# Kernel tuning notes

Hardware: AMD Instinct MI355X
Metric: run time of the kernel (lower is better)

Reference implementation:

```python
import jax, jax.numpy as jnp
import numpy as np

ED = 1024
NH = 16
HD = ED // NH


def setup_inputs() -> dict:
    key = jax.random.key(0)
    ks = jax.random.split(key, 9)
    s = 1.0 / np.sqrt(ED)
    return {
        "x": jax.random.normal(ks[0], (2, 2048, ED), dtype=jnp.float32),
        "wq": jax.random.uniform(ks[1], (ED, ED), jnp.float32, -s, s),
        "bq": jax.random.uniform(ks[2], (ED,), jnp.float32, -s, s),
        "wk": jax.random.uniform(ks[3], (ED, ED), jnp.float32, -s, s),
        "bk": jax.random.uniform(ks[4], (ED,), jnp.float32, -s, s),
        "wv": jax.random.uniform(ks[5], (ED, ED), jnp.float32, -s, s),
        "bv": jax.random.uniform(ks[6], (ED,), jnp.float32, -s, s),
        "wo": jax.random.uniform(ks[7], (ED, ED), jnp.float32, -s, s),
        "bo": jax.random.uniform(ks[8], (ED,), jnp.float32, -s, s),
    }


def reference(x, wq, bq, wk, bk, wv, bv, wo, bo):
    B, N, _ = x.shape
    # projections; weights stored as [out, in] like nn.Linear -> x @ W.T + b
    def proj(w, b):
        y = jnp.einsum('bnd,ed->bne', x, w) + b
        return y.reshape(B, N, NH, HD).transpose(0, 2, 1, 3)  # [B, H, N, hd]
    Q, K, V = proj(wq, bq), proj(wk, bk), proj(wv, bv)
    scores = jnp.einsum('bhnd,bhmd->bhnm', Q, K) / jnp.sqrt(jnp.float32(HD))
    attn = jax.nn.softmax(scores, axis=-1)
    ctx = jnp.einsum('bhnm,bhmd->bhnd', attn, V)
    ctx = ctx.transpose(0, 2, 1, 3).reshape(B, N, ED)
    return jnp.einsum('bne,de->bnd', ctx, wo) + bo
```

## Files before the change

### kernel.cpp

```cpp
#include <hip/hip_runtime.h>
#include <hip/hip_bf16.h>

#define ED 1024
#define NH 16
#define HD 64
#define SEQ 2048

typedef float f32x4 __attribute__((ext_vector_type(4)));
typedef short s16x8 __attribute__((ext_vector_type(8)));
typedef short s16x4 __attribute__((ext_vector_type(4)));
typedef __attribute__((address_space(1))) const unsigned int GBuf;
typedef __attribute__((address_space(3))) unsigned int LBuf;

#define QSC 0.18033688011112042f

union BF8 { s16x8 v; __hip_bfloat16 h[8]; };

__device__ inline void cvt_one(const float* __restrict__ s, __hip_bfloat16* __restrict__ d,
                               int n, int t, int stride) {
  const int n8 = n >> 3;
  for (int i = t; i < n8; i += stride) {
    const float4 u = ((const float4*)s)[2 * i];
    const float4 v = ((const float4*)s)[2 * i + 1];
    BF8 o;
    o.h[0] = __float2bfloat16(u.x); o.h[1] = __float2bfloat16(u.y);
    o.h[2] = __float2bfloat16(u.z); o.h[3] = __float2bfloat16(u.w);
    o.h[4] = __float2bfloat16(v.x); o.h[5] = __float2bfloat16(v.y);
    o.h[6] = __float2bfloat16(v.z); o.h[7] = __float2bfloat16(v.w);
    ((s16x8*)d)[i] = o.v;
  }
}

__global__ __launch_bounds__(256) void cvt5(const float* s0, const float* s1, const float* s2,
                                            const float* s3, const float* s4,
                                            __hip_bfloat16* d0, __hip_bfloat16* d1,
                                            __hip_bfloat16* d2, __hip_bfloat16* d3,
                                            __hip_bfloat16* d4,
                                            int n0, int n1, int n2, int n3, int n4) {
  const int stride = gridDim.x * blockDim.x;
  const int t = blockIdx.x * blockDim.x + threadIdx.x;
  cvt_one(s0, d0, n0, t, stride);
  cvt_one(s1, d1, n1, t, stride);
  cvt_one(s2, d2, n2, t, stride);
  cvt_one(s3, d3, n3, t, stride);
  cvt_one(s4, d4, n4, t, stride);
}

__global__ __launch_bounds__(256) void gemm_qkv(const __hip_bfloat16* __restrict__ A,
                                                const __hip_bfloat16* __restrict__ wq,
                                                const float* __restrict__ bq,
                                                const __hip_bfloat16* __restrict__ wk,
                                                const float* __restrict__ bk,
                                                const __hip_bfloat16* __restrict__ wv,
                                                const float* __restrict__ bv,
                                                __hip_bfloat16* __restrict__ Qo,
                                                __hip_bfloat16* __restrict__ Ko,
                                                __hip_bfloat16* __restrict__ Vo) {
  __shared__ __hip_bfloat16 As[128 * 64];
  __shared__ __hip_bfloat16 Bs[128 * 64];

  const int z = blockIdx.z;
  const __hip_bfloat16* W = (z == 0) ? wq : (z == 1) ? wk : wv;
  const float* bias = (z == 0) ? bq : (z == 1) ? bk : bv;

  const int tid = threadIdx.x;
  const int wave = tid >> 6, lane = tid & 63;
  const int ln15 = lane & 15, lg = lane >> 4;
  const int m0 = blockIdx.y * 128, n0 = blockIdx.x * 128;
  const int wr = (wave >> 1) * 64, wc = (wave & 1) * 64;

  f32x4 acc[4][4];
#pragma unroll
  for (int i = 0; i < 4; i++)
#pragma unroll
    for (int j = 0; j < 4; j++) acc[i][j] = (f32x4){0.f, 0.f, 0.f, 0.f};

  const int srow = tid >> 3;
  const int sk = (tid & 7) * 8;

  for (int k0 = 0; k0 < ED; k0 += 64) {
    __syncthreads();
#pragma unroll
    for (int c = 0; c < 4; c++) {
      const int r = c * 32 + srow;
      __builtin_amdgcn_global_load_lds((GBuf*)(A + (size_t)(m0 + r) * ED + k0 + sk),
                                       (LBuf*)((char*)As + c * 4096 + tid * 16), 16, 0, 0);
    }
#pragma unroll
    for (int c = 0; c < 4; c++) {
      const int r = c * 32 + srow;
      __builtin_amdgcn_global_load_lds((GBuf*)(W + (size_t)(n0 + r) * ED + k0 + sk),
                                       (LBuf*)((char*)Bs + c * 4096 + tid * 16), 16, 0, 0);
    }
    __syncthreads();
#pragma unroll
    for (int kb = 0; kb < 2; kb++) {
      const int kof = kb * 32 + lg * 8;
      s16x8 a[4], b[4];
#pragma unroll
      for (int i = 0; i < 4; i++)
        a[i] = *(const s16x8*)&As[(wr + i * 16 + ln15) * 64 + kof];
#pragma unroll
      for (int j = 0; j < 4; j++)
        b[j] = *(const s16x8*)&Bs[(wc + j * 16 + ln15) * 64 + kof];
#pragma unroll
      for (int i = 0; i < 4; i++)
#pragma unroll
        for (int j = 0; j < 4; j++)
          acc[i][j] = __builtin_amdgcn_mfma_f32_16x16x32_bf16(a[i], b[j], acc[i][j], 0, 0, 0);
    }
  }

  const float scale = (z == 0) ? QSC : 1.0f;
  if (z < 2) {
    __hip_bfloat16* out = (z == 0) ? Qo : Ko;
#pragma unroll
    for (int j = 0; j < 4; j++) {
      const int e = n0 + wc + j * 16 + ln15;
      const float bvv = bias[e];
      const int h = e >> 6, hd = e & 63;
#pragma unroll
      for (int i = 0; i < 4; i++) {
#pragma unroll
        for (int r = 0; r < 4; r++) {
          const int m = m0 + wr + i * 16 + lg * 4 + r;
          const int b = m >> 11, n = m & 2047;
          out[(((size_t)(b * NH + h)) * SEQ + n) * HD + hd] =
              __float2bfloat16((acc[i][j][r] + bvv) * scale);
        }
      }
    }
  } else {
#pragma unroll
    for (int j = 0; j < 4; j++) {
      const int e = n0 + wc + j * 16 + ln15;
      const float bvv = bias[e];
      const int h = e >> 6, hd = e & 63;
#pragma unroll
      for (int i = 0; i < 4; i++) {
        const int m = m0 + wr + i * 16 + lg * 4;
        const int b = m >> 11, n = m & 2047;
        union { s16x4 v; __hip_bfloat16 hh[4]; } pk;
#pragma unroll
        for (int r = 0; r < 4; r++) pk.hh[r] = __float2bfloat16(acc[i][j][r] + bvv);
        *(s16x4*)&Vo[(((size_t)(b * NH + h)) * HD + hd) * SEQ + n] = pk.v;
      }
    }
  }
}

__global__ __launch_bounds__(256) void gemm_out(const __hip_bfloat16* __restrict__ A,
                                                const __hip_bfloat16* __restrict__ W,
                                                const float* __restrict__ bias,
                                                float* __restrict__ out) {
  __shared__ __hip_bfloat16 As[128 * 64];
  __shared__ __hip_bfloat16 Bs[128 * 64];

  const int tid = threadIdx.x;
  const int wave = tid >> 6, lane = tid & 63;
  const int ln15 = lane & 15, lg = lane >> 4;
  const int m0 = blockIdx.y * 128, n0 = blockIdx.x * 128;
  const int wr = (wave >> 1) * 64, wc = (wave & 1) * 64;

  f32x4 acc[4][4];
#pragma unroll
  for (int i = 0; i < 4; i++)
#pragma unroll
    for (int j = 0; j < 4; j++) acc[i][j] = (f32x4){0.f, 0.f, 0.f, 0.f};

  const int srow = tid >> 3;
  const int sk = (tid & 7) * 8;

  for (int k0 = 0; k0 < ED; k0 += 64) {
    __syncthreads();
#pragma unroll
    for (int c = 0; c < 4; c++) {
      const int r = c * 32 + srow;
      __builtin_amdgcn_global_load_lds((GBuf*)(A + (size_t)(m0 + r) * ED + k0 + sk),
                                       (LBuf*)((char*)As + c * 4096 + tid * 16), 16, 0, 0);
    }
#pragma unroll
    for (int c = 0; c < 4; c++) {
      const int r = c * 32 + srow;
      __builtin_amdgcn_global_load_lds((GBuf*)(W + (size_t)(n0 + r) * ED + k0 + sk),
                                       (LBuf*)((char*)Bs + c * 4096 + tid * 16), 16, 0, 0);
    }
    __syncthreads();
#pragma unroll
    for (int kb = 0; kb < 2; kb++) {
      const int kof = kb * 32 + lg * 8;
      s16x8 a[4], b[4];
#pragma unroll
      for (int i = 0; i < 4; i++)
        a[i] = *(const s16x8*)&As[(wr + i * 16 + ln15) * 64 + kof];
#pragma unroll
      for (int j = 0; j < 4; j++)
        b[j] = *(const s16x8*)&Bs[(wc + j * 16 + ln15) * 64 + kof];
#pragma unroll
      for (int i = 0; i < 4; i++)
#pragma unroll
        for (int j = 0; j < 4; j++)
          acc[i][j] = __builtin_amdgcn_mfma_f32_16x16x32_bf16(a[i], b[j], acc[i][j], 0, 0, 0);
    }
  }

#pragma unroll
  for (int j = 0; j < 4; j++) {
    const int e = n0 + wc + j * 16 + ln15;
    const float bvv = bias[e];
#pragma unroll
    for (int i = 0; i < 4; i++)
#pragma unroll
      for (int r = 0; r < 4; r++) {
        const int m = m0 + wr + i * 16 + lg * 4 + r;
        out[(size_t)m * ED + e] = acc[i][j][r] + bvv;
      }
  }
}

__global__ __launch_bounds__(256) void attn_bf16(const __hip_bfloat16* __restrict__ Q,
                                                 const __hip_bfloat16* __restrict__ K,
                                                 const __hip_bfloat16* __restrict__ VT,
                                                 __hip_bfloat16* __restrict__ CTX) {
  __shared__ __hip_bfloat16 Ks[64 * 64];
  __shared__ __hip_bfloat16 Vt[64 * 64];
  __shared__ __hip_bfloat16 Ps[4 * 32 * 64];

  const int tid = threadIdx.x;
  const int wave = tid >> 6, lane = tid & 63;
  const int ln15 = lane & 15, lg = lane >> 4;
  const unsigned swz = (unsigned)((ln15 & 7) << 4);

  const int bid = blockIdx.x;
  const int work = (bid & 7) * 64 + (bid >> 3);
  const int qb = work & 15;
  const int bh = work >> 4;

  const __hip_bfloat16* Qh = Q + (size_t)bh * SEQ * HD;
  const __hip_bfloat16* Kh = K + (size_t)bh * SEQ * HD;
  const __hip_bfloat16* Vh = VT + (size_t)bh * HD * SEQ;
  __hip_bfloat16* Pw = Ps + wave * 32 * 64;

  s16x8 aq[2][2];
#pragma unroll
  for (int qs = 0; qs < 2; qs++) {
    const int qrow = qb * 128 + wave * 32 + qs * 16 + ln15;
#pragma unroll
    for (int kb = 0; kb < 2; kb++)
      aq[qs][kb] = *(const s16x8*)&Qh[(size_t)qrow * HD + kb * 32 + lg * 8];
  }

  f32x4 acc_o[2][4];
#pragma unroll
  for (int qs = 0; qs < 2; qs++)
#pragma unroll
    for (int db = 0; db < 4; db++) acc_o[qs][db] = (f32x4){0.f, 0.f, 0.f, 0.f};
  float m_[2] = {-1e30f, -1e30f};
  float l_[2] = {0.f, 0.f};

  for (int kt = 0; kt < SEQ / 64; kt++) {
    __syncthreads();
#pragma unroll
    for (int c = 0; c < 2; c++) {
      const int row = c * 32 + (tid >> 3);
      const int colb = ((tid & 7) * 16) ^ ((row & 7) << 4);
      __builtin_amdgcn_global_load_lds(
          (GBuf*)((const char*)Kh + ((size_t)(kt * 64 + row) * HD) * 2 + colb),
          (LBuf*)((char*)Ks + c * 4096 + tid * 16), 16, 0, 0);
      __builtin_amdgcn_global_load_lds(
          (GBuf*)((const char*)Vh + ((size_t)row * SEQ + kt * 64) * 2 + colb),
          (LBuf*)((char*)Vt + c * 4096 + tid * 16), 16, 0, 0);
    }
    __syncthreads();

    f32x4 s[2][4];
#pragma unroll
    for (int qs = 0; qs < 2; qs++)
#pragma unroll
      for (int cb = 0; cb < 4; cb++) s[qs][cb] = (f32x4){0.f, 0.f, 0.f, 0.f};
#pragma unroll
    for (int cb = 0; cb < 4; cb++) {
      const int krow = cb * 16 + ln15;
#pragma unroll
      for (int kb = 0; kb < 2; kb++) {
        const s16x8 ak =
            *(const s16x8*)((const char*)Ks + krow * 128 + ((kb * 64 + lg * 16) ^ swz));
#pragma unroll
        for (int qs = 0; qs < 2; qs++)
          s[qs][cb] = __builtin_amdgcn_mfma_f32_16x16x32_bf16(ak, aq[qs][kb], s[qs][cb], 0, 0, 0);
      }
    }

#pragma unroll
    for (int qs = 0; qs < 2; qs++) {
      float tm = -1e30f;
#pragma unroll
      for (int cb = 0; cb < 4; cb++)
        tm = fmaxf(tm, fmaxf(fmaxf(s[qs][cb][0], s[qs][cb][1]),
                             fmaxf(s[qs][cb][2], s[qs][cb][3])));
      tm = fmaxf(tm, __shfl_xor(tm, 16));
      tm = fmaxf(tm, __shfl_xor(tm, 32));
      const float mnew = fmaxf(m_[qs], tm);
      const float fs = exp2f(m_[qs] - mnew);
      m_[qs] = mnew;
      float sum = 0.f;
#pragma unroll
      for (int cb = 0; cb < 4; cb++)
#pragma unroll
        for (int r = 0; r < 4; r++) {
          const float p = exp2f(s[qs][cb][r] - mnew);
          s[qs][cb][r] = p;
          sum += p;
        }
      sum += __shfl_xor(sum, 16);
      sum += __shfl_xor(sum, 32);
      l_[qs] = l_[qs] * fs + sum;
#pragma unroll
      for (int db = 0; db < 4; db++)
#pragma unroll
        for (int r = 0; r < 4; r++) acc_o[qs][db][r] *= fs;
      const int prow = qs * 16 + ln15;
#pragma unroll
      for (int cb = 0; cb < 4; cb++)
#pragma unroll
        for (int r = 0; r < 4; r++) {
          const int kv2 = (cb * 16 + lg * 4 + r) * 2;
          *(__hip_bfloat16*)((char*)Pw + prow * 128 + (kv2 ^ swz)) =
              __float2bfloat16(s[qs][cb][r]);
        }
    }

#pragma unroll
    for (int kb = 0; kb < 2; kb++) {
      s16x8 bp[2];
#pragma unroll
      for (int qs = 0; qs < 2; qs++) {
        const int prow = qs * 16 + ln15;
        bp[qs] = *(const s16x8*)((const char*)Pw + prow * 128 + ((kb * 64 + lg * 16) ^ swz));
      }
#pragma unroll
      for (int db = 0; db < 4; db++) {
        const int vrow = db * 16 + ln15;
        const s16x8 av =
            *(const s16x8*)((const char*)Vt + vrow * 128 + ((kb * 64 + lg * 16) ^ swz));
#pragma unroll
        for (int qs = 0; qs < 2; qs++)
          acc_o[qs][db] = __builtin_amdgcn_mfma_f32_16x16x32_bf16(av, bp[qs], acc_o[qs][db], 0, 0, 0);
      }
    }
  }

  const int b = bh / NH, h = bh % NH;
#pragma unroll
  for (int qs = 0; qs < 2; qs++) {
    const float inv = 1.0f / l_[qs];
    const int n = qb * 128 + wave * 32 + qs * 16 + ln15;
    __hip_bfloat16* dst = &CTX[((size_t)(b * SEQ + n)) * ED + h * HD + lg * 4];
#pragma unroll
    for (int db = 0; db < 4; db++) {
      union { s16x4 v; __hip_bfloat16 hh[4]; } pk;
#pragma unroll
      for (int r = 0; r < 4; r++) pk.hh[r] = __float2bfloat16(acc_o[qs][db][r] * inv);
      *(s16x4*)&dst[db * 16] = pk.v;
    }
  }
}

extern "C" void kernel_launch(void* const* d_in, const int* in_sizes, int n_in,
                              void* d_out, int out_size, void* d_ws, size_t ws_size,
                              hipStream_t stream) {
  const float* x = (const float*)d_in[0];
  const float* wq = (const float*)d_in[1];
  const float* bq = (const float*)d_in[2];
  const float* wk = (const float*)d_in[3];
  const float* bk = (const float*)d_in[4];
  const float* wv = (const float*)d_in[5];
  const float* bv = (const float*)d_in[6];
  const float* wo = (const float*)d_in[7];
  const float* bo = (const float*)d_in[8];
  float* out = (float*)d_out;

  const int BN = in_sizes[0] / ED;

  char* w = (char*)d_ws;
  __hip_bfloat16* xbf = (__hip_bfloat16*)(w);
  __hip_bfloat16* wqb = (__hip_bfloat16*)(w + (8 << 20));
  __hip_bfloat16* wkb = (__hip_bfloat16*)(w + (10 << 20));
  __hip_bfloat16* wvb = (__hip_bfloat16*)(w + (12 << 20));
  __hip_bfloat16* wob = (__hip_bfloat16*)(w + (14 << 20));
  __hip_bfloat16* Qb = (__hip_bfloat16*)(w + (16 << 20));
  __hip_bfloat16* Kb = (__hip_bfloat16*)(w + (24 << 20));
  __hip_bfloat16* VTb = (__hip_bfloat16*)(w + (32 << 20));
  __hip_bfloat16* CTXb = (__hip_bfloat16*)(w + (40 << 20));

  cvt5<<<1024, 256, 0, stream>>>(x, wq, wk, wv, wo, xbf, wqb, wkb, wvb, wob,
                                 BN * ED, ED * ED, ED * ED, ED * ED, ED * ED);

  const dim3 blk(256);
  gemm_qkv<<<dim3(ED / 128, BN / 128, 3), blk, 0, stream>>>(
      xbf, wqb, bq, wkb, bk, wvb, bv, Qb, Kb, VTb);

  attn_bf16<<<dim3(512), blk, 0, stream>>>(Qb, Kb, VTb, CTXb);

  gemm_out<<<dim3(ED / 128, BN / 128), blk, 0, stream>>>(CTXb, wob, bo, out);
}
```

Measured before the change: 263.6 us.

## Rewrite attention inner loop with 32x32 MFMA, register P, double-buffered K/V

The attention kernel switches from 16x16x32 to 32x32x16 bf16 MFMA tiles. The softmax probabilities are packed into B-fragments in registers with v_cvt_pk_bf16 and v_permlane32_swap instead of a round trip through LDS. K/V tiles are now double-buffered so the next tile's global-to-LDS load overlaps compute, which removes one barrier per iteration. Rescaling of the running max is skipped unless the max grows by more than 8 (a lazy rescale), which trades a little numerical headroom for fewer multiplies on the accumulators.

```diff
diff --git a/kernel.cpp b/kernel.cpp
--- a/kernel.cpp
+++ b/kernel.cpp
@@ -7,6 +7,7 @@
 #define SEQ 2048
 
 typedef float f32x4 __attribute__((ext_vector_type(4)));
+typedef float f32x16 __attribute__((ext_vector_type(16)));
 typedef short s16x8 __attribute__((ext_vector_type(8)));
 typedef short s16x4 __attribute__((ext_vector_type(4)));
 typedef __attribute__((address_space(1))) const unsigned int GBuf;
@@ -15,6 +16,23 @@
 #define QSC 0.18033688011112042f
 
 union BF8 { s16x8 v; __hip_bfloat16 h[8]; };
+
+__device__ __forceinline__ unsigned cvt_pk_bf16(float lo, float hi) {
+  unsigned r;
+  asm("v_cvt_pk_bf16_f32 %0, %1, %2" : "=v"(r) : "v"(lo), "v"(hi));
+  return r;
+}
+
+__device__ __forceinline__ s16x8 pack_pfrag(float p0, float p1, float p2, float p3,
+                                            float p4, float p5, float p6, float p7) {
+  unsigned w0 = cvt_pk_bf16(p0, p1), w1 = cvt_pk_bf16(p2, p3);
+  unsigned w2 = cvt_pk_bf16(p4, p5), w3 = cvt_pk_bf16(p6, p7);
+  asm("v_permlane32_swap_b32 %0, %1" : "+v"(w0), "+v"(w2));
+  asm("v_permlane32_swap_b32 %0, %1" : "+v"(w1), "+v"(w3));
+  union { unsigned u[4]; s16x8 v; } r;
+  r.u[0] = w0; r.u[1] = w1; r.u[2] = w2; r.u[3] = w3;
+  return r.v;
+}
 
 __device__ inline void cvt_one(const float* __restrict__ s, __hip_bfloat16* __restrict__ d,
                                int n, int t, int stride) {
@@ -222,14 +240,13 @@
                                                  const __hip_bfloat16* __restrict__ K,
                                                  const __hip_bfloat16* __restrict__ VT,
                                                  __hip_bfloat16* __restrict__ CTX) {
-  __shared__ __hip_bfloat16 Ks[64 * 64];
-  __shared__ __hip_bfloat16 Vt[64 * 64];
-  __shared__ __hip_bfloat16 Ps[4 * 32 * 64];
+  __shared__ __hip_bfloat16 KsS[2][64 * 64];
+  __shared__ __hip_bfloat16 VtS[2][64 * 64];
 
   const int tid = threadIdx.x;
   const int wave = tid >> 6, lane = tid & 63;
-  const int ln15 = lane & 15, lg = lane >> 4;
-  const unsigned swz = (unsigned)((ln15 & 7) << 4);
+  const int l31 = lane & 31, hi = lane >> 5;
+  const int rswz = l31 & 7;
 
   const int bid = blockIdx.x;
   const int work = (bid & 7) * 64 + (bid >> 3);
@@ -239,130 +256,108 @@
   const __hip_bfloat16* Qh = Q + (size_t)bh * SEQ * HD;
   const __hip_bfloat16* Kh = K + (size_t)bh * SEQ * HD;
   const __hip_bfloat16* Vh = VT + (size_t)bh * HD * SEQ;
-  __hip_bfloat16* Pw = Ps + wave * 32 * 64;
-
-  s16x8 aq[2][2];
-#pragma unroll
-  for (int qs = 0; qs < 2; qs++) {
-    const int qrow = qb * 128 + wave * 32 + qs * 16 + ln15;
-#pragma unroll
-    for (int kb = 0; kb < 2; kb++)
-      aq[qs][kb] = *(const s16x8*)&Qh[(size_t)qrow * HD + kb * 32 + lg * 8];
-  }
-
-  f32x4 acc_o[2][4];
-#pragma unroll
-  for (int qs = 0; qs < 2; qs++)
-#pragma unroll
-    for (int db = 0; db < 4; db++) acc_o[qs][db] = (f32x4){0.f, 0.f, 0.f, 0.f};
-  float m_[2] = {-1e30f, -1e30f};
-  float l_[2] = {0.f, 0.f};
-
-  for (int kt = 0; kt < SEQ / 64; kt++) {
-    __syncthreads();
+
+  const int q0 = qb * 128 + wave * 32;
+
+  s16x8 aq[4];
+#pragma unroll
+  for (int kb = 0; kb < 4; kb++)
+    aq[kb] = *(const s16x8*)&Qh[(size_t)(q0 + l31) * HD + kb * 16 + hi * 8];
+
+  f32x16 acc0 = {}, acc1 = {};
+  float m_ = -1e30f, l_ = 0.f;
+
+  auto STAGE = [&](int kt_, int buf_) {
 #pragma unroll
     for (int c = 0; c < 2; c++) {
       const int row = c * 32 + (tid >> 3);
       const int colb = ((tid & 7) * 16) ^ ((row & 7) << 4);
       __builtin_amdgcn_global_load_lds(
-          (GBuf*)((const char*)Kh + ((size_t)(kt * 64 + row) * HD) * 2 + colb),
-          (LBuf*)((char*)Ks + c * 4096 + tid * 16), 16, 0, 0);
+          (GBuf*)((const char*)Kh + ((size_t)(kt_ * 64 + row) * HD) * 2 + colb),
+          (LBuf*)((char*)&KsS[buf_][0] + c * 4096 + tid * 16), 16, 0, 0);
       __builtin_amdgcn_global_load_lds(
-          (GBuf*)((const char*)Vh + ((size_t)row * SEQ + kt * 64) * 2 + colb),
-          (LBuf*)((char*)Vt + c * 4096 + tid * 16), 16, 0, 0);
-    }
+          (GBuf*)((const char*)Vh + ((size_t)row * SEQ + kt_ * 64) * 2 + colb),
+          (LBuf*)((char*)&VtS[buf_][0] + c * 4096 + tid * 16), 16, 0, 0);
+    }
+  };
+
+  STAGE(0, 0);
+
+  const int NT = SEQ / 64;
+  for (int kt = 0; kt < NT; kt++) {
+    const int cur = kt & 1;
     __syncthreads();
-
-    f32x4 s[2][4];
-#pragma unroll
-    for (int qs = 0; qs < 2; qs++)
-#pragma unroll
-      for (int cb = 0; cb < 4; cb++) s[qs][cb] = (f32x4){0.f, 0.f, 0.f, 0.f};
-#pragma unroll
-    for (int cb = 0; cb < 4; cb++) {
-      const int krow = cb * 16 + ln15;
-#pragma unroll
-      for (int kb = 0; kb < 2; kb++) {
-        const s16x8 ak =
-            *(const s16x8*)((const char*)Ks + krow * 128 + ((kb * 64 + lg * 16) ^ swz));
-#pragma unroll
-        for (int qs = 0; qs < 2; qs++)
-          s[qs][cb] = __builtin_amdgcn_mfma_f32_16x16x32_bf16(ak, aq[qs][kb], s[qs][cb], 0, 0, 0);
-      }
-    }
-
-#pragma unroll
-    for (int qs = 0; qs < 2; qs++) {
-      float tm = -1e30f;
-#pragma unroll
-      for (int cb = 0; cb < 4; cb++)
-        tm = fmaxf(tm, fmaxf(fmaxf(s[qs][cb][0], s[qs][cb][1]),
-                             fmaxf(s[qs][cb][2], s[qs][cb][3])));
-      tm = fmaxf(tm, __shfl_xor(tm, 16));
-      tm = fmaxf(tm, __shfl_xor(tm, 32));
-      const float mnew = fmaxf(m_[qs], tm);
-      const float fs = exp2f(m_[qs] - mnew);
-      m_[qs] = mnew;
-      float sum = 0.f;
-#pragma unroll
-      for (int cb = 0; cb < 4; cb++)
-#pragma unroll
-        for (int r = 0; r < 4; r++) {
-          const float p = exp2f(s[qs][cb][r] - mnew);
-          s[qs][cb][r] = p;
-          sum += p;
-        }
-      sum += __shfl_xor(sum, 16);
-      sum += __shfl_xor(sum, 32);
-      l_[qs] = l_[qs] * fs + sum;
-#pragma unroll
-      for (int db = 0; db < 4; db++)
-#pragma unroll
-        for (int r = 0; r < 4; r++) acc_o[qs][db][r] *= fs;
-      const int prow = qs * 16 + ln15;
-#pragma unroll
-      for (int cb = 0; cb < 4; cb++)
-#pragma unroll
-        for (int r = 0; r < 4; r++) {
-          const int kv2 = (cb * 16 + lg * 4 + r) * 2;
-          *(__hip_bfloat16*)((char*)Pw + prow * 128 + (kv2 ^ swz)) =
-              __float2bfloat16(s[qs][cb][r]);
-        }
-    }
-
-#pragma unroll
-    for (int kb = 0; kb < 2; kb++) {
-      s16x8 bp[2];
-#pragma unroll
-      for (int qs = 0; qs < 2; qs++) {
-        const int prow = qs * 16 + ln15;
-        bp[qs] = *(const s16x8*)((const char*)Pw + prow * 128 + ((kb * 64 + lg * 16) ^ swz));
-      }
-#pragma unroll
-      for (int db = 0; db < 4; db++) {
-        const int vrow = db * 16 + ln15;
-        const s16x8 av =
-            *(const s16x8*)((const char*)Vt + vrow * 128 + ((kb * 64 + lg * 16) ^ swz));
-#pragma unroll
-        for (int qs = 0; qs < 2; qs++)
-          acc_o[qs][db] = __builtin_amdgcn_mfma_f32_16x16x32_bf16(av, bp[qs], acc_o[qs][db], 0, 0, 0);
-      }
-    }
-  }
-
+    if (kt + 1 < NT) STAGE(kt + 1, cur ^ 1);
+
+    f32x16 s0 = {}, s1 = {};
+#pragma unroll
+    for (int kb = 0; kb < 4; kb++) {
+      const int coff = ((kb * 2 + hi) ^ rswz) << 4;
+      const s16x8 ak0 = *(const s16x8*)((const char*)&KsS[cur][0] + l31 * 128 + coff);
+      const s16x8 ak1 = *(const s16x8*)((const char*)&KsS[cur][0] + (32 + l31) * 128 + coff);
+      s0 = __builtin_amdgcn_mfma_f32_32x32x16_bf16(ak0, aq[kb], s0, 0, 0, 0);
+      s1 = __builtin_amdgcn_mfma_f32_32x32x16_bf16(ak1, aq[kb], s1, 0, 0, 0);
+    }
+
+    float t8[8];
+#pragma unroll
+    for (int i = 0; i < 8; i++)
+      t8[i] = fmaxf(fmaxf(s0[i], s0[i + 8]), fmaxf(s1[i], s1[i + 8]));
+    float tm = fmaxf(fmaxf(fmaxf(t8[0], t8[1]), fmaxf(t8[2], t8[3])),
+                     fmaxf(fmaxf(t8[4], t8[5]), fmaxf(t8[6], t8[7])));
+    tm = fmaxf(tm, __shfl_xor(tm, 32));
+
+    if (!__all(tm - m_ <= 8.0f)) {
+      const float mnew = fmaxf(m_, tm);
+      const float fs = exp2f(m_ - mnew);
+      m_ = mnew;
+      l_ *= fs;
+#pragma unroll
+      for (int r = 0; r < 16; r++) { acc0[r] *= fs; acc1[r] *= fs; }
+    }
+
+#pragma unroll
+    for (int r = 0; r < 16; r++) {
+      s0[r] = exp2f(s0[r] - m_);
+      s1[r] = exp2f(s1[r] - m_);
+    }
+    float sa[8];
+#pragma unroll
+    for (int i = 0; i < 8; i++) sa[i] = (s0[i] + s0[i + 8]) + (s1[i] + s1[i + 8]);
+    float sum = ((sa[0] + sa[1]) + (sa[2] + sa[3])) + ((sa[4] + sa[5]) + (sa[6] + sa[7]));
+    sum += __shfl_xor(sum, 32);
+    l_ += sum;
+
+    s16x8 pa[4];
+    pa[0] = pack_pfrag(s0[0], s0[1], s0[2], s0[3], s0[4], s0[5], s0[6], s0[7]);
+    pa[1] = pack_pfrag(s0[8], s0[9], s0[10], s0[11], s0[12], s0[13], s0[14], s0[15]);
+    pa[2] = pack_pfrag(s1[0], s1[1], s1[2], s1[3], s1[4], s1[5], s1[6], s1[7]);
+    pa[3] = pack_pfrag(s1[8], s1[9], s1[10], s1[11], s1[12], s1[13], s1[14], s1[15]);
+
+#pragma unroll
+    for (int kp = 0; kp < 4; kp++) {
+      const int coff = ((kp * 2 + hi) ^ rswz) << 4;
+      const s16x8 av0 = *(const s16x8*)((const char*)&VtS[cur][0] + l31 * 128 + coff);
+      const s16x8 av1 = *(const s16x8*)((const char*)&VtS[cur][0] + (32 + l31) * 128 + coff);
+      acc0 = __builtin_amdgcn_mfma_f32_32x32x16_bf16(av0, pa[kp], acc0, 0, 0, 0);
+      acc1 = __builtin_amdgcn_mfma_f32_32x32x16_bf16(av1, pa[kp], acc1, 0, 0, 0);
+    }
+  }
+
+  const float inv = 1.0f / l_;
   const int b = bh / NH, h = bh % NH;
-#pragma unroll
-  for (int qs = 0; qs < 2; qs++) {
-    const float inv = 1.0f / l_[qs];
-    const int n = qb * 128 + wave * 32 + qs * 16 + ln15;
-    __hip_bfloat16* dst = &CTX[((size_t)(b * SEQ + n)) * ED + h * HD + lg * 4];
-#pragma unroll
-    for (int db = 0; db < 4; db++) {
-      union { s16x4 v; __hip_bfloat16 hh[4]; } pk;
-#pragma unroll
-      for (int r = 0; r < 4; r++) pk.hh[r] = __float2bfloat16(acc_o[qs][db][r] * inv);
-      *(s16x4*)&dst[db * 16] = pk.v;
-    }
+  const int n = q0 + l31;
+  __hip_bfloat16* dst = &CTX[((size_t)(b * SEQ + n)) * ED + h * HD];
+#pragma unroll
+  for (int g = 0; g < 4; g++) {
+    union { s16x4 v; __hip_bfloat16 hh[4]; } p0, p1;
+#pragma unroll
+    for (int r = 0; r < 4; r++) {
+      p0.hh[r] = __float2bfloat16(acc0[4 * g + r] * inv);
+      p1.hh[r] = __float2bfloat16(acc1[4 * g + r] * inv);
+    }
+    *(s16x4*)&dst[8 * g + 4 * hi] = p0.v;
+    *(s16x4*)&dst[32 + 8 * g + 4 * hi] = p1.v;
   }
 }
 
```

Measured after the change: 243.8 us. 7.5% less time.
